# Kernel tuning notes

Measured on AMD Instinct MI355X. Metric: run time of the kernel, lower is better.

The kernel has to match this reference:

```python
import jax, jax.numpy as jnp
import numpy as np
from jax import lax

ORDER = 6
SAMPLES = 64
TOPK = 512
STRIDE = 2          # contour features are stride-2 w.r.t. input ('1' level)
NMS_THRESH = 0.2
REF_ITERS = 4
REF_MARGIN = 3.0
HC = WC = 256       # contour-feature grid
HF = WF = 512       # full-res (refinement) grid


def conv2d(x, w, b=None, pad=0):
    # x: [B,C,H,W], w: [O,I,kh,kw]
    y = lax.conv_general_dilated(x, w, (1, 1), [(pad, pad), (pad, pad)],
                                 dimension_numbers=("NCHW", "OIHW", "NCHW"))
    if b is not None:
        y = y + b[None, :, None, None]
    return y


def setup_inputs() -> dict:
    key = jax.random.key(0)
    ks = jax.random.split(key, 16)
    s = 0.05
    d = {
        "contour_features": jax.random.normal(ks[0], (4, 64, HC, WC), jnp.float32),
        "enc_score_features": jax.random.normal(ks[1], (4, 64, HC, WC), jnp.float32),
        "refinement_features": jax.random.normal(ks[2], (4, 32, HF, WF), jnp.float32),
        "enc_refinement_features": jax.random.normal(ks[3], (4, 32, HF, WF), jnp.float32),
        # learned params
        "w_score_reduce": jax.random.normal(ks[4], (64, 128, 1, 1)) * s,
        "w_score": jax.random.normal(ks[5], (2, 64, 7, 7)) * s,
        "b_score": jnp.zeros((2,), jnp.float32),
        "w_loc": jax.random.normal(ks[6], (2, 64, 7, 7)) * s,
        "b_loc": jnp.zeros((2,), jnp.float32),
        "w_fourier": jax.random.normal(ks[7], (ORDER * 4, 64, 7, 7)) * s,
        "b_fourier": jnp.zeros((ORDER * 4,), jnp.float32),
        "w_ref_reduce": jax.random.normal(ks[8], (32, 64, 1, 1)) * s,
        "w_ref": jax.random.normal(ks[9], (2, 32, 7, 7)) * s,
        "b_ref": jnp.zeros((2,), jnp.float32),
    }
    return d


def _pairwise_iou(boxes):
    # boxes: [K,4] as (x1,y1,x2,y2)
    x1, y1, x2, y2 = boxes[:, 0], boxes[:, 1], boxes[:, 2], boxes[:, 3]
    area = jnp.maximum(x2 - x1, 0.) * jnp.maximum(y2 - y1, 0.)
    ix1 = jnp.maximum(x1[:, None], x1[None, :])
    iy1 = jnp.maximum(y1[:, None], y1[None, :])
    ix2 = jnp.minimum(x2[:, None], x2[None, :])
    iy2 = jnp.minimum(y2[:, None], y2[None, :])
    inter = jnp.maximum(ix2 - ix1, 0.) * jnp.maximum(iy2 - iy1, 0.)
    union = area[:, None] + area[None, :] - inter
    return inter / jnp.maximum(union, 1e-8)


def _nms_keep(boxes, valid):
    # boxes sorted by descending score. Sequential greedy NMS.
    iou = _pairwise_iou(boxes)  # [K,K]
    idx = jnp.arange(TOPK)

    def body(i, keep):
        sup = (iou[i] > NMS_THRESH) & keep[i] & (idx > i)
        return keep & ~sup

    keep = lax.fori_loop(0, TOPK, body, valid)
    return keep


def _forward(contour_features, enc_score_features, refinement_features,
             enc_refinement_features, w_score_reduce, w_score, b_score,
             w_loc, b_loc, w_fourier, b_fourier, w_ref_reduce, w_ref, b_ref):
    B = contour_features.shape[0]
    # ---- dense heads (CPNCore.forward) ----
    sf = conv2d(jnp.concatenate([contour_features, enc_score_features], 1), w_score_reduce)
    score_logits = conv2d(sf, w_score, b_score, pad=3)            # [B,2,HC,WC]
    log_scores = jax.nn.log_softmax(score_logits, axis=1)
    locations = conv2d(contour_features, w_loc, b_loc, pad=3)     # [B,2,HC,WC]
    fourier = conv2d(contour_features, w_fourier, b_fourier, pad=3)  # [B,4*ORDER,HC,WC]

    rf = conv2d(jnp.concatenate([refinement_features, enc_refinement_features], 1), w_ref_reduce)
    refinement = jnp.tanh(conv2d(rf, w_ref, b_ref, pad=3)) * REF_MARGIN  # [B,2,HF,WF]

    # ---- proposal selection: top-K foreground scores ----
    fg = jnp.exp(log_scores[:, 1])                                # [B,HC,WC]
    fg_flat = fg.reshape(B, -1)
    top_scores, top_idx = lax.top_k(fg_flat, TOPK)                # [B,K] sorted desc
    valid = top_scores > 0.5                                      # score_thresh

    gy = (top_idx // WC).astype(jnp.float32)
    gx = (top_idx % WC).astype(jnp.float32)

    def gather_ch(t):  # t: [B,C,HC,WC] -> [B,K,C]
        C = t.shape[1]
        tf = t.reshape(B, C, -1)
        out = jnp.take_along_axis(tf, top_idx[:, None, :].repeat(C, axis=1), axis=2)
        return out.transpose(0, 2, 1)

    loc = gather_ch(locations)                                    # [B,K,2] (x,y offsets)
    fr = gather_ch(fourier).reshape(B, TOPK, ORDER, 4)            # a_x,b_x,a_y,b_y

    cx = (gx + loc[..., 0]) * STRIDE
    cy = (gy + loc[..., 1]) * STRIDE

    # ---- fourier -> contour sampling ----
    t = jnp.arange(SAMPLES, dtype=jnp.float32) / SAMPLES
    k = jnp.arange(1, ORDER + 1, dtype=jnp.float32)
    ang = 2.0 * jnp.pi * k[:, None] * t[None, :]                  # [ORDER,SAMPLES]
    cos, sin = jnp.cos(ang), jnp.sin(ang)
    px = jnp.einsum('bko,os->bks', fr[..., 0], cos) + jnp.einsum('bko,os->bks', fr[..., 1], sin)
    py = jnp.einsum('bko,os->bks', fr[..., 2], cos) + jnp.einsum('bko,os->bks', fr[..., 3], sin)
    contour = jnp.stack([px * STRIDE + cx[..., None], py * STRIDE + cy[..., None]], -1)  # [B,K,S,2]

    # ---- iterative local refinement (nearest-neighbor gather) ----
    ref_flat = refinement.reshape(B, 2, -1)
    for _ in range(REF_ITERS):
        xi = jnp.clip(jnp.round(contour[..., 0]), 0, WF - 1).astype(jnp.int32)
        yi = jnp.clip(jnp.round(contour[..., 1]), 0, HF - 1).astype(jnp.int32)
        flat = (yi * WF + xi).reshape(B, 1, -1)                   # [B,1,K*S]
        off = jnp.take_along_axis(ref_flat, flat.repeat(2, axis=1), axis=2)
        off = off.reshape(B, 2, TOPK, SAMPLES).transpose(0, 2, 3, 1)  # [B,K,S,2]
        contour = contour + off

    # ---- boxes + NMS ----
    boxes = jnp.concatenate([contour.min(axis=2), contour.max(axis=2)], -1)  # [B,K,4]
    keep = jax.vmap(_nms_keep)(boxes, valid)
    return contour, top_scores, keep, boxes


def reference(contour_features, enc_score_features, refinement_features,
              enc_refinement_features, w_score_reduce, w_score, b_score,
              w_loc, b_loc, w_fourier, b_fourier, w_ref_reduce, w_ref, b_ref):
    return _forward(contour_features, enc_score_features, refinement_features,
                    enc_refinement_features, w_score_reduce, w_score, b_score,
                    w_loc, b_loc, w_fourier, b_fourier, w_ref_reduce, w_ref, b_ref)
```

## Files before the change

kernel.cpp:

```cpp
#include <hip/hip_runtime.h>
#include <math.h>

#define WS_D     0ull
#define WS_REF   1048576ull
#define WS_SPART 9437184ull
#define WS_WSE   13631488ull
#define WS_WRE   13731840ull
#define WS_WG    13782016ull
#define WS_TIDX  14108160ull
#define WS_GATH  14116352ull
#define WS_TRIG  14329344ull
#define WS_CLIST 14332416ull
#define WS_CNT   14365184ull
#define WS_PAIRS 14365200ull
#define WS_WRE32 14430736ull
#define WS_WSE32 14455824ull
#define WS_END   14506000ull

__global__ __launch_bounds__(256) void cpn_prep_kernel(
    const float* __restrict__ w_score_reduce, const float* __restrict__ w_score,
    const float* __restrict__ w_loc, const float* __restrict__ w_fourier,
    const float* __restrict__ w_ref_reduce, const float* __restrict__ w_ref,
    double* __restrict__ wse, double* __restrict__ wre, float* __restrict__ wg,
    float* __restrict__ trig, float* __restrict__ wre32, float* __restrict__ wse32)
{
    int i = blockIdx.x * 256 + threadIdx.x;
    if (i < 12544) {
        int o = i / 6272;
        int rem = i % 6272;
        int c = rem / 49, r = rem % 49;
        double a = 0.0;
        for (int m = 0; m < 64; ++m)
            a += (double)w_score[(o*64 + m)*49 + r] * (double)w_score_reduce[m*128 + c];
        wse[i] = a;
    } else if (i < 12544 + 6272) {
        int t = i - 12544;
        int o = t / 3136;
        int rem = t % 3136;
        int c = rem / 49, r = rem % 49;
        double a = 0.0;
        for (int m = 0; m < 32; ++m)
            a += (double)w_ref[(o*32 + m)*49 + r] * (double)w_ref_reduce[m*64 + c];
        wre[t] = a;
    } else if (i < 12544 + 6272 + 81536) {
        int t = i - 18816;
        int tap = t / 26, o = t % 26;
        wg[t] = (o < 2) ? w_loc[o*3136 + tap] : w_fourier[(o - 2)*3136 + tap];
    } else if (i < 100352 + 768) {
        int t = i - 100352;
        int cs = t / 384;
        int k = (t % 384) / 64, s = t % 64;
        const float TWO_PI_F = (float)6.283185307179586;
        float a1 = TWO_PI_F * (float)(k + 1);
        float tf = (float)s * 0.015625f;
        float ang = a1 * tf;
        double av = (double)ang;
        trig[t] = (cs == 0) ? (float)cos(av) : (float)sin(av);
    } else if (i < 101120 + 6272) {
        int t = i - 101120;
        int c = t / 98, r98 = t % 98;
        int ky = r98 / 14, q = r98 % 14;
        int kx = q >> 1, o = q & 1;
        int rr = ky*7 + kx;
        double a = 0.0;
        for (int m = 0; m < 32; ++m)
            a += (double)w_ref[(o*32 + m)*49 + rr] * (double)w_ref_reduce[m*64 + c];
        wre32[t] = (float)a;
    } else if (i < 107392 + 12544) {
        int t = i - 107392;
        int c = t / 98, r98 = t % 98;
        int ky = r98 / 14, q = r98 % 14;
        int kx = q >> 1, o = q & 1;
        int rr = ky*7 + kx;
        double a = 0.0;
        for (int m = 0; m < 64; ++m)
            a += (double)w_score[(o*64 + m)*49 + rr] * (double)w_score_reduce[m*128 + c];
        wse32[t] = (float)a;
    }
}

__global__ __launch_bounds__(512) void cpn_score_dense_kernel(
    const float* __restrict__ cf, const float* __restrict__ esf,
    const float* __restrict__ wse32, float2* __restrict__ partial)
{
    __shared__ __align__(16) float spatch[2][1672];
    const int tid  = threadIdx.x;
    const int t2   = tid & 255;
    const int h    = tid >> 8;
    const int b    = blockIdx.z >> 1;
    const int srch = blockIdx.z & 1;
    const float* src = srch ? esf : cf;
    const float* sbase = src + ((size_t)(b*64 + h*32) << 16);
    const int row0 = blockIdx.y * 32;
    const int col0 = blockIdx.x * 32;
    const int ty   = t2 >> 3;
    const int txg  = t2 & 7;
    const int cbase = srch*64 + h*32;

    float acc0[4] = {0.f,0.f,0.f,0.f};
    float acc1[4] = {0.f,0.f,0.f,0.f};
    float sreg[6];

    {
        #pragma unroll
        for (int k = 0; k < 6; ++k) {
            int i = k*256 + t2; float v = 0.f;
            if (i < 1520) {
                int r = i/40, j = i%40;
                int gy = row0 - 3 + r, gx = col0 - 4 + j;
                if ((unsigned)gy < 256u && (unsigned)gx < 256u) v = sbase[gy*256 + gx];
            }
            sreg[k] = v;
        }
    }

    for (int c = 0; c < 32; ++c) {
        #pragma unroll
        for (int k = 0; k < 6; ++k) {
            int i = k*256 + t2;
            if (i < 1520) spatch[h][(i/40)*44 + (i%40)] = sreg[k];
        }
        __syncthreads();
        if (c + 1 < 32) {
            const float* sp = sbase + ((size_t)(c+1) << 16);
            #pragma unroll
            for (int k = 0; k < 6; ++k) {
                int i = k*256 + t2; float v = 0.f;
                if (i < 1520) {
                    int r = i/40, j = i%40;
                    int gy = row0 - 3 + r, gx = col0 - 4 + j;
                    if ((unsigned)gy < 256u && (unsigned)gx < 256u) v = sp[gy*256 + gx];
                }
                sreg[k] = v;
            }
        }
        int cg = __builtin_amdgcn_readfirstlane(cbase + c);
        const float* wc = wse32 + cg*98;
        #pragma unroll
        for (int ky = 0; ky < 7; ++ky) {
            const float4* pr4 = reinterpret_cast<const float4*>(&spatch[h][(ty+ky)*44 + txg*4]);
            float4 A = pr4[0], B2 = pr4[1], C2 = pr4[2];
            float rv[12] = {A.x,A.y,A.z,A.w,B2.x,B2.y,B2.z,B2.w,C2.x,C2.y,C2.z,C2.w};
            const float* wp = wc + ky*14;
            float wv[14];
            #pragma unroll
            for (int q = 0; q < 14; ++q) wv[q] = wp[q];
            #pragma unroll
            for (int kx = 0; kx < 7; ++kx) {
                float w0 = wv[2*kx], w1 = wv[2*kx+1];
                #pragma unroll
                for (int p = 0; p < 4; ++p) {
                    float v = rv[p + kx + 1];
                    acc0[p] = fmaf(w0, v, acc0[p]);
                    acc1[p] = fmaf(w1, v, acc1[p]);
                }
            }
        }
        __syncthreads();
    }

    float* cmb = &spatch[0][0];
    if (h == 1) {
        #pragma unroll
        for (int p = 0; p < 4; ++p) { cmb[t2*8 + p] = acc0[p]; cmb[t2*8 + 4 + p] = acc1[p]; }
    }
    __syncthreads();
    if (h == 0) {
        int y = row0 + ty;
        #pragma unroll
        for (int p = 0; p < 4; ++p) {
            float s0 = acc0[p] + cmb[t2*8 + p];
            float s1 = acc1[p] + cmb[t2*8 + 4 + p];
            int x = col0 + txg*4 + p;
            float2 v; v.x = s0; v.y = s1;
            partial[(size_t)(srch*4 + b)*65536 + y*256 + x] = v;
        }
    }
}

__global__ __launch_bounds__(256) void cpn_dcomb_kernel(
    const float2* __restrict__ partial, float* __restrict__ d)
{
    int i = blockIdx.x * 256 + threadIdx.x;
    int b = i >> 16, px = i & 65535;
    float2 p0 = partial[(size_t)b*65536 + px];
    float2 p1 = partial[(size_t)(4 + b)*65536 + px];
    float l0 = p0.x + p1.x;
    float l1 = p0.y + p1.y;
    d[i] = l1 - l0;
}

__global__ __launch_bounds__(512) void cpn_ref_conv_kernel(
    const float* __restrict__ rff, const float* __restrict__ erf,
    const float* __restrict__ wre32, const float* __restrict__ b_ref,
    float* __restrict__ refmap)
{
    __shared__ __align__(16) float4 patches[2][38][19];
    const int tid = threadIdx.x;
    const int t2  = tid & 255;
    const int h   = tid >> 8;
    const int b   = blockIdx.z;
    const int row0 = blockIdx.y * 32;
    const int col0 = blockIdx.x * 64;
    const int tyg = t2 & 31;
    const int txg = t2 >> 5;
    const float* sbase = (h ? erf : rff) + ((size_t)(b*32) << 18);

    int   st_r[3], st_f[3];
    long  st_off[3];
    bool  st_ok[3];
    #pragma unroll
    for (int k = 0; k < 3; ++k) {
        int i = k*256 + t2;
        int r = i / 18, f = i % 18;
        int gy = row0 - 3 + r, gx = col0 - 4 + 4*f;
        st_r[k] = r; st_f[k] = f;
        st_ok[k] = (i < 684) && ((unsigned)gy < 512u) && ((unsigned)gx < 509u);
        st_off[k] = (long)gy * 512 + gx;
    }

    float4 s4[3];
    {
        #pragma unroll
        for (int k = 0; k < 3; ++k) {
            float4 v = {0.f,0.f,0.f,0.f};
            if (st_ok[k]) v = *reinterpret_cast<const float4*>(sbase + st_off[k]);
            s4[k] = v;
        }
    }

    float acc0[8] = {0,0,0,0,0,0,0,0};
    float acc1[8] = {0,0,0,0,0,0,0,0};

    for (int c = 0; c < 32; ++c) {
        #pragma unroll
        for (int k = 0; k < 3; ++k) {
            int i = k*256 + t2;
            if (i < 684) patches[h][st_r[k]][st_f[k]] = s4[k];
        }
        __syncthreads();
        if (c + 1 < 32) {
            const float* sp = sbase + ((size_t)(c+1) << 18);
            #pragma unroll
            for (int k = 0; k < 3; ++k) {
                float4 v = {0.f,0.f,0.f,0.f};
                if (st_ok[k]) v = *reinterpret_cast<const float4*>(sp + st_off[k]);
                s4[k] = v;
            }
        }
        int cg = __builtin_amdgcn_readfirstlane(h*32 + c);
        const float* wc = wre32 + cg*98;
        #pragma unroll
        for (int pr = 0; pr < 7; ++pr) {
            int row = tyg + pr;
            float4 A  = patches[h][row][2*txg + 0];
            float4 B2 = patches[h][row][2*txg + 1];
            float4 C2 = patches[h][row][2*txg + 2];
            float4 D2 = patches[h][row][2*txg + 3];
            float rv[16] = {A.x,A.y,A.z,A.w,B2.x,B2.y,B2.z,B2.w,
                            C2.x,C2.y,C2.z,C2.w,D2.x,D2.y,D2.z,D2.w};
            const float* wp = wc + pr*14;
            float wv[14];
            #pragma unroll
            for (int q = 0; q < 14; ++q) wv[q] = wp[q];
            #pragma unroll
            for (int kx = 0; kx < 7; ++kx) {
                float w0 = wv[2*kx], w1 = wv[2*kx+1];
                #pragma unroll
                for (int p = 0; p < 8; ++p) {
                    float v = rv[p + kx + 1];
                    acc0[p] = fmaf(w0, v, acc0[p]);
                    acc1[p] = fmaf(w1, v, acc1[p]);
                }
            }
        }
        __syncthreads();
    }

    float* cmb = reinterpret_cast<float*>(&patches[0][0][0]);
    if (h == 1) {
        #pragma unroll
        for (int p = 0; p < 8; ++p) { cmb[t2*16 + p] = acc0[p]; cmb[t2*16 + 8 + p] = acc1[p]; }
    }
    __syncthreads();
    if (h == 0) {
        float br0 = b_ref[0], br1 = b_ref[1];
        int y = row0 + tyg;
        int x0 = col0 + txg*8;
        #pragma unroll
        for (int p = 0; p < 8; ++p) {
            float s0 = acc0[p] + cmb[t2*16 + p];
            float s1 = acc1[p] + cmb[t2*16 + 8 + p];
            refmap[((size_t)(b*2 + 0)*512 + y)*512 + x0 + p] = tanhf(s0 + br0) * 3.0f;
            refmap[((size_t)(b*2 + 1)*512 + y)*512 + x0 + p] = tanhf(s1 + br1) * 3.0f;
        }
    }
}

__device__ __forceinline__ void cpn_find_bucket(
    unsigned int* hist, unsigned int* seg, int nb, int target, int tid,
    int* s_bsel, int* s_cnt)
{
    int nseg = nb / 32;
    for (int t = tid; t < nseg; t += 1024) {
        unsigned int s = 0;
        for (int q = 0; q < 32; ++q) s += hist[t*32 + q];
        seg[t] = s;
    }
    __syncthreads();
    if (tid == 0) {
        int cum = 0, sg = 0;
        for (int jj = nseg - 1; jj >= 0; --jj) {
            int c = (int)seg[jj];
            if (cum + c >= target) { sg = jj; break; }
            cum += c;
        }
        int bs = sg*32;
        for (int jj = sg*32 + 31; jj >= sg*32; --jj) {
            int c = (int)hist[jj];
            if (cum + c >= target) { bs = jj; break; }
            cum += c;
        }
        *s_bsel = bs; *s_cnt = cum;
    }
    __syncthreads();
}

__device__ __forceinline__ unsigned int cpn_fkey(float v) {
    unsigned int u = __float_as_uint(v);
    return (u & 0x80000000u) ? ~u : (u | 0x80000000u);
}

__global__ __launch_bounds__(1024) void cpn_select_kernel(
    const float* __restrict__ d, int* __restrict__ clist, int* __restrict__ cnt)
{
    const int b = blockIdx.x;
    const int tid = threadIdx.x;
    const float* f = d + (size_t)b * 65536;

    __shared__ unsigned int hist[2048];
    __shared__ unsigned int seg[64];
    __shared__ int s_b, s_c, s_n;

    const int bitsA[3]  = {11,11,10};
    const int shiftA[3] = {21,10,0};

    unsigned int prefix = 0;
    int target = 512;
    for (int pass = 0; pass < 3; ++pass) {
        int sh = shiftA[pass], nb = 1 << bitsA[pass];
        for (int i = tid; i < 2048; i += 1024) hist[i] = 0;
        __syncthreads();
        if (pass == 0) {
            for (int i = tid; i < 65536; i += 1024) {
                unsigned int k = cpn_fkey(f[i]);
                atomicAdd(&hist[k >> 21], 1u);
            }
        } else {
            int hs = sh + bitsA[pass];
            for (int i = tid; i < 65536; i += 1024) {
                unsigned int k = cpn_fkey(f[i]);
                if ((k >> hs) == prefix)
                    atomicAdd(&hist[(k >> sh) & (nb-1)], 1u);
            }
        }
        __syncthreads();
        cpn_find_bucket(hist, seg, nb, target, tid, &s_b, &s_c);
        prefix = (prefix << bitsA[pass]) | (unsigned)s_b;
        target -= s_c;
    }
    float T = (prefix & 0x80000000u) ? __uint_as_float(prefix & 0x7FFFFFFFu)
                                     : __uint_as_float(~prefix);
    float tval = T - 0.0625f;

    if (tid == 0) s_n = 0;
    __syncthreads();
    for (int i = tid; i < 65536; i += 1024) {
        if (f[i] >= tval) {
            int q = atomicAdd(&s_n, 1);
            if (q < 2048) clist[b*2048 + q] = i;
        }
    }
    __syncthreads();
    if (tid == 0) cnt[b] = (s_n > 2048) ? 2048 : s_n;
}

__global__ __launch_bounds__(256) void cpn_recompute_kernel(
    const float* __restrict__ cf, const float* __restrict__ esf,
    const double* __restrict__ wse, const float* __restrict__ b_score,
    const int* __restrict__ clist, const int* __restrict__ cnt,
    uint2* __restrict__ pairs)
{
    const int b = blockIdx.y, q = blockIdx.x, tid = threadIdx.x;
    const int n = cnt[b];
    if (q >= n) {
        if (tid == 0) { uint2 pd; pd.x = 0u; pd.y = 0x7FFFFFFFu; pairs[b*2048 + q] = pd; }
        return;
    }
    const int idx = clist[b*2048 + q];
    const int gy = idx >> 8, gx = idx & 255;

    double L0 = 0.0, L1 = 0.0;
    for (int t = tid; t < 6272; t += 256) {
        int c = t / 49, r = t % 49, ky = r / 7, kx = r % 7;
        int y = gy + ky - 3, x = gx + kx - 3;
        float v = 0.f;
        if ((unsigned)y < 256u && (unsigned)x < 256u) {
            const float* src = (c < 64) ? cf : esf;
            v = src[((size_t)(b*64 + (c & 63)) << 16) + y*256 + x];
        }
        double dv = (double)v;
        L0 = fma(dv, wse[c*49 + r], L0);
        L1 = fma(dv, wse[6272 + c*49 + r], L1);
    }
    #pragma unroll
    for (int off = 32; off; off >>= 1) {
        L0 += __shfl_down(L0, off, 64);
        L1 += __shfl_down(L1, off, 64);
    }
    __shared__ double red[4][2];
    int w = tid >> 6, lane = tid & 63;
    if (lane == 0) { red[w][0] = L0; red[w][1] = L1; }
    __syncthreads();
    if (tid == 0) {
        double S0 = red[0][0] + red[1][0] + red[2][0] + red[3][0];
        double S1 = red[0][1] + red[1][1] + red[2][1] + red[3][1];
        float l0f = (float)(S0 + (double)b_score[0]);
        float l1f = (float)(S1 + (double)b_score[1]);
        float m  = fmaxf(l0f, l1f);
        float e0 = (float)exp((double)(l0f - m));
        float e1 = (float)exp((double)(l1f - m));
        float s  = e0 + e1;
        float lg = (float)log((double)s);
        float ls1 = (l1f - m) - lg;
        float fgv = (float)exp((double)ls1);
        uint2 pr; pr.x = __float_as_uint(fgv); pr.y = (unsigned)idx;
        pairs[b*2048 + q] = pr;
    }
}

__global__ __launch_bounds__(1024) void cpn_sortk_kernel(
    const uint2* __restrict__ pairs, int* __restrict__ tidx,
    float* __restrict__ tscores)
{
    const int b = blockIdx.x;
    const int tid = threadIdx.x;
    __shared__ unsigned int key[2048];
    __shared__ int sidx[2048];

    for (int q = tid; q < 2048; q += 1024) {
        uint2 pr = pairs[b*2048 + q];
        key[q] = pr.x; sidx[q] = (int)pr.y;
    }
    __syncthreads();
    for (int kk = 2; kk <= 2048; kk <<= 1)
        for (int jj = kk >> 1; jj > 0; jj >>= 1) {
            for (int i = tid; i < 2048; i += 1024) {
                int ixj = i ^ jj;
                if (ixj > i) {
                    unsigned int ka = key[i], kc = key[ixj];
                    int ia = sidx[i], ic = sidx[ixj];
                    bool up = ((i & kk) == 0);
                    bool aBefore = (ka > kc) || (ka == kc && ia < ic);
                    if (up ? !aBefore : aBefore) {
                        key[i] = kc; key[ixj] = ka;
                        sidx[i] = ic; sidx[ixj] = ia;
                    }
                }
            }
            __syncthreads();
        }
    for (int q = tid; q < 512; q += 1024) {
        tscores[b*512 + q] = __uint_as_float(key[q]);
        tidx[b*512 + q] = sidx[q];
    }
}

__global__ __launch_bounds__(256) void cpn_gather_conv_kernel(
    const float* __restrict__ cf, const float* __restrict__ wg,
    const float* __restrict__ b_loc, const float* __restrict__ b_fourier,
    const int* __restrict__ tidx, float* __restrict__ gath)
{
    const int b = blockIdx.y, p = blockIdx.x, tid = threadIdx.x;
    const int idx = tidx[b*512 + p];
    const int gy = idx >> 8, gx = idx & 255;

    double part[26];
    #pragma unroll
    for (int o = 0; o < 26; ++o) part[o] = 0.0;

    for (int t = tid; t < 3136; t += 256) {
        int c = t / 49, rr = t % 49, ky = rr / 7, kx = rr % 7;
        int y = gy + ky - 3, x = gx + kx - 3;
        float v = 0.f;
        if ((unsigned)y < 256u && (unsigned)x < 256u)
            v = cf[((size_t)(b*64 + c)*256 + y)*256 + x];
        const float* wr = wg + t*26;
        double dv = (double)v;
        #pragma unroll
        for (int o = 0; o < 26; ++o) part[o] = fma(dv, (double)wr[o], part[o]);
    }
    #pragma unroll
    for (int o = 0; o < 26; ++o)
        for (int off = 32; off; off >>= 1) part[o] += __shfl_down(part[o], off, 64);

    __shared__ double red[4][26];
    int w = tid >> 6, lane = tid & 63;
    if (lane == 0) {
        #pragma unroll
        for (int o = 0; o < 26; ++o) red[w][o] = part[o];
    }
    __syncthreads();
    if (tid < 26) {
        double s = red[0][tid] + red[1][tid] + red[2][tid] + red[3][tid];
        s += (tid < 2) ? (double)b_loc[tid] : (double)b_fourier[tid - 2];
        gath[((size_t)b*512 + p)*26 + tid] = (float)s;
    }
}

__global__ __launch_bounds__(64) void cpn_contour_kernel(
    const float* __restrict__ gath, const int* __restrict__ tidx,
    const float* __restrict__ refmap, const float* __restrict__ trig,
    float* __restrict__ out_contour, float* __restrict__ out_boxes)
{
    const int bp = blockIdx.x;
    const int b = bp >> 9;
    const int s = threadIdx.x;
    const float* g = gath + (size_t)bp * 26;
    const int idx = tidx[bp];
    const int gy = idx >> 8, gx = idx & 255;

    float cx = ((float)gx + g[0]) * 2.0f;
    float cy = ((float)gy + g[1]) * 2.0f;

    float sxc = 0.f, sxs = 0.f, syc = 0.f, sys = 0.f;
    #pragma unroll
    for (int k = 0; k < 6; ++k) {
        float cs = trig[k*64 + s];
        float sn = trig[384 + k*64 + s];
        float t0 = g[2 + k*4 + 0] * cs; asm volatile("" : "+v"(t0)); sxc += t0;
        float t1 = g[2 + k*4 + 1] * sn; asm volatile("" : "+v"(t1)); sxs += t1;
        float t2 = g[2 + k*4 + 2] * cs; asm volatile("" : "+v"(t2)); syc += t2;
        float t3 = g[2 + k*4 + 3] * sn; asm volatile("" : "+v"(t3)); sys += t3;
    }
    float px = sxc + sxs;
    float py = syc + sys;
    float x = px * 2.0f; asm volatile("" : "+v"(x)); x += cx;
    float y = py * 2.0f; asm volatile("" : "+v"(y)); y += cy;

    const float* r0 = refmap + (size_t)b * 2 * 262144;
    const float* r1 = r0 + 262144;
    #pragma unroll
    for (int it = 0; it < 4; ++it) {
        float xr = rintf(x); xr = fminf(fmaxf(xr, 0.f), 511.f);
        float yr = rintf(y); yr = fminf(fmaxf(yr, 0.f), 511.f);
        int xi = (int)xr, yi = (int)yr;
        x += r0[yi*512 + xi];
        y += r1[yi*512 + xi];
    }

    out_contour[((size_t)bp*64 + s)*2 + 0] = x;
    out_contour[((size_t)bp*64 + s)*2 + 1] = y;

    float mnx = x, mxx = x, mny = y, mxy = y;
    #pragma unroll
    for (int off = 32; off; off >>= 1) {
        mnx = fminf(mnx, __shfl_xor(mnx, off, 64));
        mny = fminf(mny, __shfl_xor(mny, off, 64));
        mxx = fmaxf(mxx, __shfl_xor(mxx, off, 64));
        mxy = fmaxf(mxy, __shfl_xor(mxy, off, 64));
    }
    if (s == 0) {
        out_boxes[bp*4 + 0] = mnx;
        out_boxes[bp*4 + 1] = mny;
        out_boxes[bp*4 + 2] = mxx;
        out_boxes[bp*4 + 3] = mxy;
    }
}

__global__ __launch_bounds__(512) void cpn_nms_kernel(
    const float* __restrict__ boxes, const float* __restrict__ scores,
    float* __restrict__ keep_out)
{
    const int b = blockIdx.x;
    const int j = threadIdx.x;
    __shared__ float X1[512], Y1[512], X2[512], Y2[512], AR[512];
    __shared__ int keep[512];

    const float* bb = boxes + b*512*4;
    float x1 = bb[j*4+0], y1 = bb[j*4+1], x2 = bb[j*4+2], y2 = bb[j*4+3];
    float aj = fmaxf(x2 - x1, 0.f) * fmaxf(y2 - y1, 0.f);
    X1[j] = x1; Y1[j] = y1; X2[j] = x2; Y2[j] = y2; AR[j] = aj;
    keep[j] = (scores[b*512 + j] > 0.5f) ? 1 : 0;
    __syncthreads();

    for (int i = 0; i < 512; ++i) {
        if (keep[i] && j > i) {
            float ix1 = fmaxf(x1, X1[i]);
            float iy1 = fmaxf(y1, Y1[i]);
            float ix2 = fminf(x2, X2[i]);
            float iy2 = fminf(y2, Y2[i]);
            float inter = fmaxf(ix2 - ix1, 0.f) * fmaxf(iy2 - iy1, 0.f);
            float uni = (aj + AR[i]) - inter;
            float iou = inter / fmaxf(uni, 1e-8f);
            if (iou > 0.2f) keep[j] = 0;
        }
        __syncthreads();
    }
    keep_out[b*512 + j] = keep[j] ? 1.0f : 0.0f;
}

extern "C" void kernel_launch(void* const* d_in, const int* in_sizes, int n_in,
                              void* d_out, int out_size, void* d_ws, size_t ws_size,
                              hipStream_t stream)
{
    if (ws_size < WS_END) return;

    const float* cf   = (const float*)d_in[0];
    const float* esf  = (const float*)d_in[1];
    const float* rff  = (const float*)d_in[2];
    const float* erf  = (const float*)d_in[3];
    const float* w_sr = (const float*)d_in[4];
    const float* w_s  = (const float*)d_in[5];
    const float* b_s  = (const float*)d_in[6];
    const float* w_l  = (const float*)d_in[7];
    const float* b_l  = (const float*)d_in[8];
    const float* w_f  = (const float*)d_in[9];
    const float* b_f  = (const float*)d_in[10];
    const float* w_rr = (const float*)d_in[11];
    const float* w_r  = (const float*)d_in[12];
    const float* b_r  = (const float*)d_in[13];

    char* ws = (char*)d_ws;
    float*  dbuf = (float*)(ws + WS_D);
    float*  refm = (float*)(ws + WS_REF);
    float2* spart = (float2*)(ws + WS_SPART);
    double* wse  = (double*)(ws + WS_WSE);
    double* wre  = (double*)(ws + WS_WRE);
    float*  wg   = (float*)(ws + WS_WG);
    int*    tidx = (int*)(ws + WS_TIDX);
    float*  gath = (float*)(ws + WS_GATH);
    float*  trig = (float*)(ws + WS_TRIG);
    int*    clist = (int*)(ws + WS_CLIST);
    int*    cnt  = (int*)(ws + WS_CNT);
    uint2*  pairs = (uint2*)(ws + WS_PAIRS);
    float*  wre32 = (float*)(ws + WS_WRE32);
    float*  wse32 = (float*)(ws + WS_WSE32);

    float* out_contour = (float*)d_out;
    float* out_scores  = out_contour + 262144;
    float* out_keep    = out_scores + 2048;
    float* out_boxes   = out_keep + 2048;

    cpn_prep_kernel<<<dim3(469), dim3(256), 0, stream>>>(
        w_sr, w_s, w_l, w_f, w_rr, w_r, wse, wre, wg, trig, wre32, wse32);
    cpn_score_dense_kernel<<<dim3(8, 8, 8), dim3(512), 0, stream>>>(
        cf, esf, wse32, spart);
    cpn_ref_conv_kernel<<<dim3(8, 16, 4), dim3(512), 0, stream>>>(
        rff, erf, wre32, b_r, refm);
    cpn_dcomb_kernel<<<dim3(1024), dim3(256), 0, stream>>>(spart, dbuf);
    cpn_select_kernel<<<dim3(4), dim3(1024), 0, stream>>>(dbuf, clist, cnt);
    cpn_recompute_kernel<<<dim3(2048, 4), dim3(256), 0, stream>>>(
        cf, esf, wse, b_s, clist, cnt, pairs);
    cpn_sortk_kernel<<<dim3(4), dim3(1024), 0, stream>>>(pairs, tidx, out_scores);
    cpn_gather_conv_kernel<<<dim3(512, 4), dim3(256), 0, stream>>>(
        cf, wg, b_l, b_f, tidx, gath);
    cpn_contour_kernel<<<dim3(2048), dim3(64), 0, stream>>>(
        gath, tidx, refm, trig, out_contour, out_boxes);
    cpn_nms_kernel<<<dim3(4), dim3(512), 0, stream>>>(
        out_boxes, out_scores, out_keep);
}
```

Measured before the change: 673.4 us.

## Split conv channel reduction four ways with smaller row tiles, doubling grid size

Both dense conv kernels (score and refinement) now split the input-channel reduction across four 128-thread groups instead of two 256-thread groups. They use 16-row tiles instead of 32, which doubles the number of blocks launched. The score kernel also switches its halo staging to float4 vector loads. The intent is more blocks for better CU occupancy and load balance on the GPU. The cost is more halo rows reloaded per output row and a three-way shared-memory reduction at the end.

Measured after the change: 695.9 us. +3.3%, slower.

```diff
diff --git a/kernel.cpp b/kernel.cpp
--- a/kernel.cpp
+++ b/kernel.cpp
@@ -83,68 +83,73 @@
     const float* __restrict__ cf, const float* __restrict__ esf,
     const float* __restrict__ wse32, float2* __restrict__ partial)
 {
-    __shared__ __align__(16) float spatch[2][1672];
+    __shared__ __align__(16) float4 patches[4][22][11];
     const int tid  = threadIdx.x;
-    const int t2   = tid & 255;
-    const int h    = tid >> 8;
+    const int t2   = tid & 127;
+    const int q    = tid >> 7;
     const int b    = blockIdx.z >> 1;
     const int srch = blockIdx.z & 1;
     const float* src = srch ? esf : cf;
-    const float* sbase = src + ((size_t)(b*64 + h*32) << 16);
-    const int row0 = blockIdx.y * 32;
+    const float* sbase = src + ((size_t)(b*64 + q*16) << 16);
+    const int row0 = blockIdx.y * 16;
     const int col0 = blockIdx.x * 32;
-    const int ty   = t2 >> 3;
+    const int tyg  = t2 >> 3;
     const int txg  = t2 & 7;
-    const int cbase = srch*64 + h*32;
+    const int cbase = srch*64 + q*16;
+
+    int  st_r[2], st_f[2];
+    long st_off[2];
+    bool st_ok[2];
+    #pragma unroll
+    for (int k = 0; k < 2; ++k) {
+        int i = k*128 + t2;
+        int r = i / 10, f = i % 10;
+        int gy = row0 - 3 + r, gx = col0 - 4 + 4*f;
+        st_r[k] = r; st_f[k] = f;
+        st_ok[k] = (i < 220) && ((unsigned)gy < 256u) && ((unsigned)gx < 253u);
+        st_off[k] = (long)gy * 256 + gx;
+    }
+
+    float4 s4[2];
+    #pragma unroll
+    for (int k = 0; k < 2; ++k) {
+        float4 v = {0.f,0.f,0.f,0.f};
+        if (st_ok[k]) v = *reinterpret_cast<const float4*>(sbase + st_off[k]);
+        s4[k] = v;
+    }
 
     float acc0[4] = {0.f,0.f,0.f,0.f};
     float acc1[4] = {0.f,0.f,0.f,0.f};
-    float sreg[6];
-
-    {
-        #pragma unroll
-        for (int k = 0; k < 6; ++k) {
-            int i = k*256 + t2; float v = 0.f;
-            if (i < 1520) {
-                int r = i/40, j = i%40;
-                int gy = row0 - 3 + r, gx = col0 - 4 + j;
-                if ((unsigned)gy < 256u && (unsigned)gx < 256u) v = sbase[gy*256 + gx];
-            }
-            sreg[k] = v;
-        }
-    }
-
-    for (int c = 0; c < 32; ++c) {
-        #pragma unroll
-        for (int k = 0; k < 6; ++k) {
-            int i = k*256 + t2;
-            if (i < 1520) spatch[h][(i/40)*44 + (i%40)] = sreg[k];
+
+    for (int c = 0; c < 16; ++c) {
+        #pragma unroll
+        for (int k = 0; k < 2; ++k) {
+            int i = k*128 + t2;
+            if (i < 220) patches[q][st_r[k]][st_f[k]] = s4[k];
         }
         __syncthreads();
-        if (c + 1 < 32) {
+        if (c + 1 < 16) {
             const float* sp = sbase + ((size_t)(c+1) << 16);
             #pragma unroll
-            for (int k = 0; k < 6; ++k) {
-                int i = k*256 + t2; float v = 0.f;
-                if (i < 1520) {
-                    int r = i/40, j = i%40;
-                    int gy = row0 - 3 + r, gx = col0 - 4 + j;
-                    if ((unsigned)gy < 256u && (unsigned)gx < 256u) v = sp[gy*256 + gx];
-                }
-                sreg[k] = v;
+            for (int k = 0; k < 2; ++k) {
+                float4 v = {0.f,0.f,0.f,0.f};
+                if (st_ok[k]) v = *reinterpret_cast<const float4*>(sp + st_off[k]);
+                s4[k] = v;
             }
         }
         int cg = __builtin_amdgcn_readfirstlane(cbase + c);
         const float* wc = wse32 + cg*98;
         #pragma unroll
-        for (int ky = 0; ky < 7; ++ky) {
-            const float4* pr4 = reinterpret_cast<const float4*>(&spatch[h][(ty+ky)*44 + txg*4]);
-            float4 A = pr4[0], B2 = pr4[1], C2 = pr4[2];
+        for (int pr = 0; pr < 7; ++pr) {
+            int row = tyg + pr;
+            float4 A = patches[q][row][txg + 0];
+            float4 B2 = patches[q][row][txg + 1];
+            float4 C2 = patches[q][row][txg + 2];
             float rv[12] = {A.x,A.y,A.z,A.w,B2.x,B2.y,B2.z,B2.w,C2.x,C2.y,C2.z,C2.w};
-            const float* wp = wc + ky*14;
+            const float* wp = wc + pr*14;
             float wv[14];
             #pragma unroll
-            for (int q = 0; q < 14; ++q) wv[q] = wp[q];
+            for (int w = 0; w < 14; ++w) wv[w] = wp[w];
             #pragma unroll
             for (int kx = 0; kx < 7; ++kx) {
                 float w0 = wv[2*kx], w1 = wv[2*kx+1];
@@ -159,18 +164,22 @@
         __syncthreads();
     }
 
-    float* cmb = &spatch[0][0];
-    if (h == 1) {
-        #pragma unroll
-        for (int p = 0; p < 4; ++p) { cmb[t2*8 + p] = acc0[p]; cmb[t2*8 + 4 + p] = acc1[p]; }
-    }
-    __syncthreads();
-    if (h == 0) {
-        int y = row0 + ty;
+    float* cmb = reinterpret_cast<float*>(&patches[0][0][0]);
+    if (q > 0) {
+        int base = ((q-1)*128 + t2)*8;
+        #pragma unroll
+        for (int p = 0; p < 4; ++p) { cmb[base + p] = acc0[p]; cmb[base + 4 + p] = acc1[p]; }
+    }
+    __syncthreads();
+    if (q == 0) {
+        int y = row0 + tyg;
         #pragma unroll
         for (int p = 0; p < 4; ++p) {
-            float s0 = acc0[p] + cmb[t2*8 + p];
-            float s1 = acc1[p] + cmb[t2*8 + 4 + p];
+            float s0 = acc0[p];
+            float s1 = acc1[p];
+            s0 += cmb[(0*128 + t2)*8 + p];      s1 += cmb[(0*128 + t2)*8 + 4 + p];
+            s0 += cmb[(1*128 + t2)*8 + p];      s1 += cmb[(1*128 + t2)*8 + 4 + p];
+            s0 += cmb[(2*128 + t2)*8 + p];      s1 += cmb[(2*128 + t2)*8 + 4 + p];
             int x = col0 + txg*4 + p;
             float2 v; v.x = s0; v.y = s1;
             partial[(size_t)(srch*4 + b)*65536 + y*256 + x] = v;
@@ -195,74 +204,72 @@
     const float* __restrict__ wre32, const float* __restrict__ b_ref,
     float* __restrict__ refmap)
 {
-    __shared__ __align__(16) float4 patches[2][38][19];
+    __shared__ __align__(16) float4 patches[4][22][19];
     const int tid = threadIdx.x;
-    const int t2  = tid & 255;
-    const int h   = tid >> 8;
+    const int t2  = tid & 127;
+    const int q   = tid >> 7;
     const int b   = blockIdx.z;
-    const int row0 = blockIdx.y * 32;
+    const int row0 = blockIdx.y * 16;
     const int col0 = blockIdx.x * 64;
-    const int tyg = t2 & 31;
-    const int txg = t2 >> 5;
-    const float* sbase = (h ? erf : rff) + ((size_t)(b*32) << 18);
-
-    int   st_r[3], st_f[3];
-    long  st_off[3];
-    bool  st_ok[3];
-    #pragma unroll
-    for (int k = 0; k < 3; ++k) {
-        int i = k*256 + t2;
+    const int tyg = t2 & 15;
+    const int txg = t2 >> 4;
+    const float* sbase = ((q < 2) ? rff : erf) + ((size_t)(b*32 + (q & 1)*16) << 18);
+
+    int  st_r[4], st_f[4];
+    long st_off[4];
+    bool st_ok[4];
+    #pragma unroll
+    for (int k = 0; k < 4; ++k) {
+        int i = k*128 + t2;
         int r = i / 18, f = i % 18;
         int gy = row0 - 3 + r, gx = col0 - 4 + 4*f;
         st_r[k] = r; st_f[k] = f;
-        st_ok[k] = (i < 684) && ((unsigned)gy < 512u) && ((unsigned)gx < 509u);
+        st_ok[k] = (i < 396) && ((unsigned)gy < 512u) && ((unsigned)gx < 509u);
         st_off[k] = (long)gy * 512 + gx;
     }
 
-    float4 s4[3];
-    {
-        #pragma unroll
-        for (int k = 0; k < 3; ++k) {
-            float4 v = {0.f,0.f,0.f,0.f};
-            if (st_ok[k]) v = *reinterpret_cast<const float4*>(sbase + st_off[k]);
-            s4[k] = v;
-        }
+    float4 s4[4];
+    #pragma unroll
+    for (int k = 0; k < 4; ++k) {
+        float4 v = {0.f,0.f,0.f,0.f};
+        if (st_ok[k]) v = *reinterpret_cast<const float4*>(sbase + st_off[k]);
+        s4[k] = v;
     }
 
     float acc0[8] = {0,0,0,0,0,0,0,0};
     float acc1[8] = {0,0,0,0,0,0,0,0};
 
-    for (int c = 0; c < 32; ++c) {
-        #pragma unroll
-        for (int k = 0; k < 3; ++k) {
-            int i = k*256 + t2;
-            if (i < 684) patches[h][st_r[k]][st_f[k]] = s4[k];
+    for (int c = 0; c < 16; ++c) {
+        #pragma unroll
+        for (int k = 0; k < 4; ++k) {
+            int i = k*128 + t2;
+            if (i < 396) patches[q][st_r[k]][st_f[k]] = s4[k];
         }
         __syncthreads();
-        if (c + 1 < 32) {
+        if (c + 1 < 16) {
             const float* sp = sbase + ((size_t)(c+1) << 18);
             #pragma unroll
-            for (int k = 0; k < 3; ++k) {
+            for (int k = 0; k < 4; ++k) {
                 float4 v = {0.f,0.f,0.f,0.f};
                 if (st_ok[k]) v = *reinterpret_cast<const float4*>(sp + st_off[k]);
                 s4[k] = v;
             }
         }
-        int cg = __builtin_amdgcn_readfirstlane(h*32 + c);
+        int cg = __builtin_amdgcn_readfirstlane(q*16 + c);
         const float* wc = wre32 + cg*98;
         #pragma unroll
         for (int pr = 0; pr < 7; ++pr) {
             int row = tyg + pr;
-            float4 A  = patches[h][row][2*txg + 0];
-            float4 B2 = patches[h][row][2*txg + 1];
-            float4 C2 = patches[h][row][2*txg + 2];
-            float4 D2 = patches[h][row][2*txg + 3];
+            float4 A  = patches[q][row][2*txg + 0];
+            float4 B2 = patches[q][row][2*txg + 1];
+            float4 C2 = patches[q][row][2*txg + 2];
+            float4 D2 = patches[q][row][2*txg + 3];
             float rv[16] = {A.x,A.y,A.z,A.w,B2.x,B2.y,B2.z,B2.w,
                             C2.x,C2.y,C2.z,C2.w,D2.x,D2.y,D2.z,D2.w};
             const float* wp = wc + pr*14;
             float wv[14];
             #pragma unroll
-            for (int q = 0; q < 14; ++q) wv[q] = wp[q];
+            for (int w = 0; w < 14; ++w) wv[w] = wp[w];
             #pragma unroll
             for (int kx = 0; kx < 7; ++kx) {
                 float w0 = wv[2*kx], w1 = wv[2*kx+1];
@@ -278,19 +285,23 @@
     }
 
     float* cmb = reinterpret_cast<float*>(&patches[0][0][0]);
-    if (h == 1) {
-        #pragma unroll
-        for (int p = 0; p < 8; ++p) { cmb[t2*16 + p] = acc0[p]; cmb[t2*16 + 8 + p] = acc1[p]; }
-    }
-    __syncthreads();
-    if (h == 0) {
+    if (q > 0) {
+        int base = ((q-1)*128 + t2)*16;
+        #pragma unroll
+        for (int p = 0; p < 8; ++p) { cmb[base + p] = acc0[p]; cmb[base + 8 + p] = acc1[p]; }
+    }
+    __syncthreads();
+    if (q == 0) {
         float br0 = b_ref[0], br1 = b_ref[1];
         int y = row0 + tyg;
         int x0 = col0 + txg*8;
         #pragma unroll
         for (int p = 0; p < 8; ++p) {
-            float s0 = acc0[p] + cmb[t2*16 + p];
-            float s1 = acc1[p] + cmb[t2*16 + 8 + p];
+            float s0 = acc0[p];
+            float s1 = acc1[p];
+            s0 += cmb[(0*128 + t2)*16 + p];      s1 += cmb[(0*128 + t2)*16 + 8 + p];
+            s0 += cmb[(1*128 + t2)*16 + p];      s1 += cmb[(1*128 + t2)*16 + 8 + p];
+            s0 += cmb[(2*128 + t2)*16 + p];      s1 += cmb[(2*128 + t2)*16 + 8 + p];
             refmap[((size_t)(b*2 + 0)*512 + y)*512 + x0 + p] = tanhf(s0 + br0) * 3.0f;
             refmap[((size_t)(b*2 + 1)*512 + y)*512 + x0 + p] = tanhf(s1 + br1) * 3.0f;
         }
@@ -654,9 +665,9 @@
 
     cpn_prep_kernel<<<dim3(469), dim3(256), 0, stream>>>(
         w_sr, w_s, w_l, w_f, w_rr, w_r, wse, wre, wg, trig, wre32, wse32);
-    cpn_score_dense_kernel<<<dim3(8, 8, 8), dim3(512), 0, stream>>>(
+    cpn_score_dense_kernel<<<dim3(8, 16, 8), dim3(512), 0, stream>>>(
         cf, esf, wse32, spart);
-    cpn_ref_conv_kernel<<<dim3(8, 16, 4), dim3(512), 0, stream>>>(
+    cpn_ref_conv_kernel<<<dim3(8, 32, 4), dim3(512), 0, stream>>>(
         rff, erf, wre32, b_r, refm);
     cpn_dcomb_kernel<<<dim3(1024), dim3(256), 0, stream>>>(spart, dbuf);
     cpn_select_kernel<<<dim3(4), dim3(1024), 0, stream>>>(dbuf, clist, cnt);
```

## Fuse gather-conv with contour kernel, cache select keys, single-wave NMS

Applied to the files above, without the earlier changes.

Three changes. The select kernel now loads its 64 sort keys per thread into registers once, instead of re-reading global memory on every radix pass and in the final compaction. The gather-conv and contour kernels are merged so the 26 head outputs stay in shared memory, which removes one launch and a workspace round trip. NMS now runs as a single 64-thread wave per image with volatile shared keep flags and no per-iteration barrier. This leans on in-wave ordering of shared-memory writes and reads for correctness. The compaction comparison switches from floats to ordered integer keys, which could differ for NaN inputs.

Measured after the change: 744.8 us. 1.11x slower.

```diff
diff --git a/kernel.cpp b/kernel.cpp
--- a/kernel.cpp
+++ b/kernel.cpp
@@ -342,6 +342,10 @@
     __shared__ unsigned int seg[64];
     __shared__ int s_b, s_c, s_n;
 
+    unsigned int keys[64];
+    #pragma unroll
+    for (int k = 0; k < 64; ++k) keys[k] = cpn_fkey(f[tid + 1024*k]);
+
     const int bitsA[3]  = {11,11,10};
     const int shiftA[3] = {21,10,0};
 
@@ -352,16 +356,16 @@
         for (int i = tid; i < 2048; i += 1024) hist[i] = 0;
         __syncthreads();
         if (pass == 0) {
-            for (int i = tid; i < 65536; i += 1024) {
-                unsigned int k = cpn_fkey(f[i]);
-                atomicAdd(&hist[k >> 21], 1u);
-            }
+            #pragma unroll
+            for (int k = 0; k < 64; ++k)
+                atomicAdd(&hist[keys[k] >> 21], 1u);
         } else {
             int hs = sh + bitsA[pass];
-            for (int i = tid; i < 65536; i += 1024) {
-                unsigned int k = cpn_fkey(f[i]);
-                if ((k >> hs) == prefix)
-                    atomicAdd(&hist[(k >> sh) & (nb-1)], 1u);
+            #pragma unroll
+            for (int k = 0; k < 64; ++k) {
+                unsigned int kk = keys[k];
+                if ((kk >> hs) == prefix)
+                    atomicAdd(&hist[(kk >> sh) & (nb-1)], 1u);
             }
         }
         __syncthreads();
@@ -371,14 +375,15 @@
     }
     float T = (prefix & 0x80000000u) ? __uint_as_float(prefix & 0x7FFFFFFFu)
                                      : __uint_as_float(~prefix);
-    float tval = T - 0.0625f;
+    unsigned int tkey = cpn_fkey(T - 0.0625f);
 
     if (tid == 0) s_n = 0;
     __syncthreads();
-    for (int i = tid; i < 65536; i += 1024) {
-        if (f[i] >= tval) {
+    #pragma unroll
+    for (int k = 0; k < 64; ++k) {
+        if (keys[k] >= tkey) {
             int q = atomicAdd(&s_n, 1);
-            if (q < 2048) clist[b*2048 + q] = i;
+            if (q < 2048) clist[b*2048 + q] = tid + 1024*k;
         }
     }
     __syncthreads();
@@ -476,13 +481,16 @@
     }
 }
 
-__global__ __launch_bounds__(256) void cpn_gather_conv_kernel(
+__global__ __launch_bounds__(256) void cpn_gather_contour_kernel(
     const float* __restrict__ cf, const float* __restrict__ wg,
     const float* __restrict__ b_loc, const float* __restrict__ b_fourier,
-    const int* __restrict__ tidx, float* __restrict__ gath)
+    const int* __restrict__ tidx, const float* __restrict__ refmap,
+    const float* __restrict__ trig,
+    float* __restrict__ out_contour, float* __restrict__ out_boxes)
 {
     const int b = blockIdx.y, p = blockIdx.x, tid = threadIdx.x;
-    const int idx = tidx[b*512 + p];
+    const int bp = b*512 + p;
+    const int idx = tidx[bp];
     const int gy = idx >> 8, gx = idx & 255;
 
     double part[26];
@@ -505,6 +513,7 @@
         for (int off = 32; off; off >>= 1) part[o] += __shfl_down(part[o], off, 64);
 
     __shared__ double red[4][26];
+    __shared__ float g26[26];
     int w = tid >> 6, lane = tid & 63;
     if (lane == 0) {
         #pragma unroll
@@ -514,100 +523,109 @@
     if (tid < 26) {
         double s = red[0][tid] + red[1][tid] + red[2][tid] + red[3][tid];
         s += (tid < 2) ? (double)b_loc[tid] : (double)b_fourier[tid - 2];
-        gath[((size_t)b*512 + p)*26 + tid] = (float)s;
-    }
-}
-
-__global__ __launch_bounds__(64) void cpn_contour_kernel(
-    const float* __restrict__ gath, const int* __restrict__ tidx,
-    const float* __restrict__ refmap, const float* __restrict__ trig,
-    float* __restrict__ out_contour, float* __restrict__ out_boxes)
-{
-    const int bp = blockIdx.x;
-    const int b = bp >> 9;
-    const int s = threadIdx.x;
-    const float* g = gath + (size_t)bp * 26;
-    const int idx = tidx[bp];
-    const int gy = idx >> 8, gx = idx & 255;
-
-    float cx = ((float)gx + g[0]) * 2.0f;
-    float cy = ((float)gy + g[1]) * 2.0f;
-
-    float sxc = 0.f, sxs = 0.f, syc = 0.f, sys = 0.f;
-    #pragma unroll
-    for (int k = 0; k < 6; ++k) {
-        float cs = trig[k*64 + s];
-        float sn = trig[384 + k*64 + s];
-        float t0 = g[2 + k*4 + 0] * cs; asm volatile("" : "+v"(t0)); sxc += t0;
-        float t1 = g[2 + k*4 + 1] * sn; asm volatile("" : "+v"(t1)); sxs += t1;
-        float t2 = g[2 + k*4 + 2] * cs; asm volatile("" : "+v"(t2)); syc += t2;
-        float t3 = g[2 + k*4 + 3] * sn; asm volatile("" : "+v"(t3)); sys += t3;
-    }
-    float px = sxc + sxs;
-    float py = syc + sys;
-    float x = px * 2.0f; asm volatile("" : "+v"(x)); x += cx;
-    float y = py * 2.0f; asm volatile("" : "+v"(y)); y += cy;
-
-    const float* r0 = refmap + (size_t)b * 2 * 262144;
-    const float* r1 = r0 + 262144;
-    #pragma unroll
-    for (int it = 0; it < 4; ++it) {
-        float xr = rintf(x); xr = fminf(fmaxf(xr, 0.f), 511.f);
-        float yr = rintf(y); yr = fminf(fmaxf(yr, 0.f), 511.f);
-        int xi = (int)xr, yi = (int)yr;
-        x += r0[yi*512 + xi];
-        y += r1[yi*512 + xi];
-    }
-
-    out_contour[((size_t)bp*64 + s)*2 + 0] = x;
-    out_contour[((size_t)bp*64 + s)*2 + 1] = y;
-
-    float mnx = x, mxx = x, mny = y, mxy = y;
-    #pragma unroll
-    for (int off = 32; off; off >>= 1) {
-        mnx = fminf(mnx, __shfl_xor(mnx, off, 64));
-        mny = fminf(mny, __shfl_xor(mny, off, 64));
-        mxx = fmaxf(mxx, __shfl_xor(mxx, off, 64));
-        mxy = fmaxf(mxy, __shfl_xor(mxy, off, 64));
-    }
-    if (s == 0) {
-        out_boxes[bp*4 + 0] = mnx;
-        out_boxes[bp*4 + 1] = mny;
-        out_boxes[bp*4 + 2] = mxx;
-        out_boxes[bp*4 + 3] = mxy;
-    }
-}
-
-__global__ __launch_bounds__(512) void cpn_nms_kernel(
+        g26[tid] = (float)s;
+    }
+    __syncthreads();
+
+    if (tid < 64) {
+        const int s = tid;
+        const float* g = g26;
+        float cx = ((float)gx + g[0]) * 2.0f;
+        float cy = ((float)gy + g[1]) * 2.0f;
+
+        float sxc = 0.f, sxs = 0.f, syc = 0.f, sys = 0.f;
+        #pragma unroll
+        for (int k = 0; k < 6; ++k) {
+            float cs = trig[k*64 + s];
+            float sn = trig[384 + k*64 + s];
+            float t0 = g[2 + k*4 + 0] * cs; asm volatile("" : "+v"(t0)); sxc += t0;
+            float t1 = g[2 + k*4 + 1] * sn; asm volatile("" : "+v"(t1)); sxs += t1;
+            float t2 = g[2 + k*4 + 2] * cs; asm volatile("" : "+v"(t2)); syc += t2;
+            float t3 = g[2 + k*4 + 3] * sn; asm volatile("" : "+v"(t3)); sys += t3;
+        }
+        float px = sxc + sxs;
+        float py = syc + sys;
+        float x = px * 2.0f; asm volatile("" : "+v"(x)); x += cx;
+        float y = py * 2.0f; asm volatile("" : "+v"(y)); y += cy;
+
+        const float* r0 = refmap + (size_t)b * 2 * 262144;
+        const float* r1 = r0 + 262144;
+        #pragma unroll
+        for (int it = 0; it < 4; ++it) {
+            float xr = rintf(x); xr = fminf(fmaxf(xr, 0.f), 511.f);
+            float yr = rintf(y); yr = fminf(fmaxf(yr, 0.f), 511.f);
+            int xi = (int)xr, yi = (int)yr;
+            x += r0[yi*512 + xi];
+            y += r1[yi*512 + xi];
+        }
+
+        out_contour[((size_t)bp*64 + s)*2 + 0] = x;
+        out_contour[((size_t)bp*64 + s)*2 + 1] = y;
+
+        float mnx = x, mxx = x, mny = y, mxy = y;
+        #pragma unroll
+        for (int off = 32; off; off >>= 1) {
+            mnx = fminf(mnx, __shfl_xor(mnx, off, 64));
+            mny = fminf(mny, __shfl_xor(mny, off, 64));
+            mxx = fmaxf(mxx, __shfl_xor(mxx, off, 64));
+            mxy = fmaxf(mxy, __shfl_xor(mxy, off, 64));
+        }
+        if (s == 0) {
+            out_boxes[bp*4 + 0] = mnx;
+            out_boxes[bp*4 + 1] = mny;
+            out_boxes[bp*4 + 2] = mxx;
+            out_boxes[bp*4 + 3] = mxy;
+        }
+    }
+}
+
+__global__ __launch_bounds__(64) void cpn_nms_kernel(
     const float* __restrict__ boxes, const float* __restrict__ scores,
     float* __restrict__ keep_out)
 {
     const int b = blockIdx.x;
-    const int j = threadIdx.x;
+    const int t = threadIdx.x;
     __shared__ float X1[512], Y1[512], X2[512], Y2[512], AR[512];
-    __shared__ int keep[512];
-
+    __shared__ int keep_s[512];
+    volatile int* keep = keep_s;
+
+    float x1r[8], y1r[8], x2r[8], y2r[8], ar[8];
     const float* bb = boxes + b*512*4;
-    float x1 = bb[j*4+0], y1 = bb[j*4+1], x2 = bb[j*4+2], y2 = bb[j*4+3];
-    float aj = fmaxf(x2 - x1, 0.f) * fmaxf(y2 - y1, 0.f);
-    X1[j] = x1; Y1[j] = y1; X2[j] = x2; Y2[j] = y2; AR[j] = aj;
-    keep[j] = (scores[b*512 + j] > 0.5f) ? 1 : 0;
+    #pragma unroll
+    for (int k = 0; k < 8; ++k) {
+        int j = t + 64*k;
+        float x1 = bb[j*4+0], y1 = bb[j*4+1], x2 = bb[j*4+2], y2 = bb[j*4+3];
+        float aj = fmaxf(x2 - x1, 0.f) * fmaxf(y2 - y1, 0.f);
+        x1r[k] = x1; y1r[k] = y1; x2r[k] = x2; y2r[k] = y2; ar[k] = aj;
+        X1[j] = x1; Y1[j] = y1; X2[j] = x2; Y2[j] = y2; AR[j] = aj;
+        keep_s[j] = (scores[b*512 + j] > 0.5f) ? 1 : 0;
+    }
     __syncthreads();
 
     for (int i = 0; i < 512; ++i) {
-        if (keep[i] && j > i) {
-            float ix1 = fmaxf(x1, X1[i]);
-            float iy1 = fmaxf(y1, Y1[i]);
-            float ix2 = fminf(x2, X2[i]);
-            float iy2 = fminf(y2, Y2[i]);
-            float inter = fmaxf(ix2 - ix1, 0.f) * fmaxf(iy2 - iy1, 0.f);
-            float uni = (aj + AR[i]) - inter;
-            float iou = inter / fmaxf(uni, 1e-8f);
-            if (iou > 0.2f) keep[j] = 0;
-        }
-        __syncthreads();
-    }
-    keep_out[b*512 + j] = keep[j] ? 1.0f : 0.0f;
+        if (keep[i]) {
+            float bx1 = X1[i], by1 = Y1[i], bx2 = X2[i], by2 = Y2[i], ba = AR[i];
+            #pragma unroll
+            for (int k = 0; k < 8; ++k) {
+                int j = t + 64*k;
+                if (j > i && keep[j]) {
+                    float ix1 = fmaxf(x1r[k], bx1);
+                    float iy1 = fmaxf(y1r[k], by1);
+                    float ix2 = fminf(x2r[k], bx2);
+                    float iy2 = fminf(y2r[k], by2);
+                    float inter = fmaxf(ix2 - ix1, 0.f) * fmaxf(iy2 - iy1, 0.f);
+                    float uni = (ar[k] + ba) - inter;
+                    float iou = inter / fmaxf(uni, 1e-8f);
+                    if (iou > 0.2f) keep[j] = 0;
+                }
+            }
+        }
+    }
+    #pragma unroll
+    for (int k = 0; k < 8; ++k) {
+        int j = t + 64*k;
+        keep_out[b*512 + j] = keep[j] ? 1.0f : 0.0f;
+    }
 }
 
 extern "C" void kernel_launch(void* const* d_in, const int* in_sizes, int n_in,
@@ -639,7 +657,6 @@
     double* wre  = (double*)(ws + WS_WRE);
     float*  wg   = (float*)(ws + WS_WG);
     int*    tidx = (int*)(ws + WS_TIDX);
-    float*  gath = (float*)(ws + WS_GATH);
     float*  trig = (float*)(ws + WS_TRIG);
     int*    clist = (int*)(ws + WS_CLIST);
     int*    cnt  = (int*)(ws + WS_CNT);
@@ -663,10 +680,8 @@
     cpn_recompute_kernel<<<dim3(2048, 4), dim3(256), 0, stream>>>(
         cf, esf, wse, b_s, clist, cnt, pairs);
     cpn_sortk_kernel<<<dim3(4), dim3(1024), 0, stream>>>(pairs, tidx, out_scores);
-    cpn_gather_conv_kernel<<<dim3(512, 4), dim3(256), 0, stream>>>(
-        cf, wg, b_l, b_f, tidx, gath);
-    cpn_contour_kernel<<<dim3(2048), dim3(64), 0, stream>>>(
-        gath, tidx, refm, trig, out_contour, out_boxes);
-    cpn_nms_kernel<<<dim3(4), dim3(512), 0, stream>>>(
+    cpn_gather_contour_kernel<<<dim3(512, 4), dim3(256), 0, stream>>>(
+        cf, wg, b_l, b_f, tidx, refm, trig, out_contour, out_boxes);
+    cpn_nms_kernel<<<dim3(4), dim3(64), 0, stream>>>(
         out_boxes, out_scores, out_keep);
 }
```
